# Kernel tuning notes

Hardware: AMD Instinct MI355X
Metric: run time of the kernel (lower is better)

## Reference

```python
import jax, jax.numpy as jnp
import numpy as np

B, C, K = 16384, 10, 5   # batch, context window (2*window_size), num_neg per context
V, D = 400000, 300       # vocab size, embedding dim


def setup_inputs() -> dict:
    key = jax.random.key(0)
    k1, k2, k3, k4, k5 = jax.random.split(key, 5)
    return {
        "target": jax.random.randint(k1, (B,), 0, V, dtype=jnp.int64)
        if jax.config.jax_enable_x64 else jax.random.randint(k1, (B,), 0, V).astype(jnp.int32),
        "context": jax.random.randint(k2, (B, C), 0, V).astype(jnp.int32),
        "negative_samples": jax.random.randint(k3, (B, C * K), 0, V).astype(jnp.int32),
        "emb_in": jax.random.normal(k4, (V, D), dtype=jnp.float32),
        "emb_out": jax.random.normal(k5, (V, D), dtype=jnp.float32),
    }


def reference(target, context, negative_samples, emb_in, emb_out):
    # Skip-gram NCE loss (Word2VecPy.loss).
    tgt = emb_in[target]               # [B, D]
    ctx = emb_out[context]             # [B, C, D]
    neg = emb_out[negative_samples]    # [B, C*K, D]

    # positive: log sigmoid(ctx . tgt), mean over context
    pos_scores = jnp.einsum("bcd,bd->bc", ctx, tgt)          # [B, C]
    pos_loss = jnp.mean(jax.nn.log_sigmoid(pos_scores), axis=1)  # [B]

    # negative: log sigmoid(-neg . tgt), sum over K negatives, mean over context
    neg_scores = -jnp.einsum("bnd,bd->bn", neg, tgt)         # [B, C*K]
    neg_ls = jax.nn.log_sigmoid(neg_scores).reshape(B, C, K)  # [B, C, K]
    neg_loss = jnp.mean(jnp.sum(neg_ls, axis=2), axis=1)      # [B]

    return -jnp.mean(pos_loss + neg_loss)
```

## Files before the change

### kernel.cpp

```cpp
#include <hip/hip_runtime.h>
#include <hip/hip_bf16.h>


#define D_DIM 300
#define D4    75
#define C_DIM 10
#define NEG_DIM 50
#define ROWS 60

__device__ __forceinline__ float log_sigmoid_fast(float x) {
    float e = __expf(-fabsf(x));
    return fminf(x, 0.f) - __logf(1.f + e);
}

__global__ __launch_bounds__(256) void w2v_loss_partial(
    const int*   __restrict__ target,
    const int*   __restrict__ context,
    const int*   __restrict__ negs,
    const float* __restrict__ emb_in,
    const float* __restrict__ emb_out,
    float*       __restrict__ partial)
{
    const int b    = blockIdx.x;
    const int tid  = threadIdx.x;
    const int lane = tid & 63;
    const int wave = tid >> 6;

    __shared__ int   s_idx[ROWS + 4];
    __shared__ float s_acc[4];

    if (tid < C_DIM)       s_idx[tid] = context[b * C_DIM + tid];
    else if (tid < ROWS)   s_idx[tid] = negs[b * NEG_DIM + (tid - C_DIM)];
    __syncthreads();

    const float4* trow =
        reinterpret_cast<const float4*>(emb_in + (size_t)target[b] * D_DIM);
    float4 ta = trow[lane];
    float4 tb = make_float4(0.f, 0.f, 0.f, 0.f);
    if (lane < D4 - 64) tb = trow[64 + lane];

    float acc = 0.f;
    #pragma unroll 3
    for (int rr = 0; rr < ROWS / 4; ++rr) {
        const int r   = wave + rr * 4;
        const int idx = s_idx[r];
        const float4* row =
            reinterpret_cast<const float4*>(emb_out + (size_t)idx * D_DIM);
        float4 ra = row[lane];
        float4 rb = make_float4(0.f, 0.f, 0.f, 0.f);
        if (lane < D4 - 64) rb = row[64 + lane];

        float dot = ra.x * ta.x + ra.y * ta.y + ra.z * ta.z + ra.w * ta.w
                  + rb.x * tb.x + rb.y * tb.y + rb.z * tb.z + rb.w * tb.w;

        #pragma unroll
        for (int off = 32; off > 0; off >>= 1)
            dot += __shfl_xor(dot, off, 64);

        const float x = (r < C_DIM) ? dot : -dot;
        acc += log_sigmoid_fast(x);
    }

    if (lane == 0) s_acc[wave] = acc;
    __syncthreads();
    if (tid == 0) partial[b] = s_acc[0] + s_acc[1] + s_acc[2] + s_acc[3];
}

__global__ __launch_bounds__(256) void w2v_loss_reduce(
    const float* __restrict__ partial,
    float*       __restrict__ out,
    int n, float inv_scale)
{
    __shared__ float s[256];
    float acc = 0.f;
    for (int i = threadIdx.x; i < n; i += 256) acc += partial[i];
    s[threadIdx.x] = acc;
    __syncthreads();
    #pragma unroll
    for (int off = 128; off > 0; off >>= 1) {
        if (threadIdx.x < off) s[threadIdx.x] += s[threadIdx.x + off];
        __syncthreads();
    }
    if (threadIdx.x == 0) out[0] = -s[0] * inv_scale;
}

extern "C" void kernel_launch(void* const* d_in, const int* in_sizes, int n_in,
                              void* d_out, int out_size, void* d_ws, size_t ws_size,
                              hipStream_t stream) {
    const int*   target  = (const int*)  d_in[0];
    const int*   context = (const int*)  d_in[1];
    const int*   negs    = (const int*)  d_in[2];
    const float* emb_in  = (const float*)d_in[3];
    const float* emb_out = (const float*)d_in[4];
    float*       out     = (float*)d_out;

    const int B = in_sizes[0];
    float* partial = (float*)d_ws;

    w2v_loss_partial<<<B, 256, 0, stream>>>(target, context, negs,
                                            emb_in, emb_out, partial);
    const float inv_scale = 1.0f / ((float)B * (float)C_DIM);
    w2v_loss_reduce<<<1, 256, 0, stream>>>(partial, out, B, inv_scale);
}
```

Before: 210.6 us.

## Map one batch item per wave and batch shuffle reductions across four rows

Each wavefront now processes a whole batch item, with four items per block, instead of splitting one item's rows across four waves. Context and negative indices are held in lane registers and broadcast with readlane, which removes the shared-memory staging and block barriers. Four dot products are reduced together with a combined butterfly, cutting the shuffle count per row. The trade-off is more independent loads per wave and a slightly more intricate lane-to-row mapping.

```diff
diff --git a/kernel.cpp b/kernel.cpp
--- a/kernel.cpp
+++ b/kernel.cpp
@@ -21,49 +21,61 @@
     const float* __restrict__ emb_out,
     float*       __restrict__ partial)
 {
-    const int b    = blockIdx.x;
     const int tid  = threadIdx.x;
     const int lane = tid & 63;
     const int wave = tid >> 6;
+    const int b    = blockIdx.x * 4 + wave;
 
-    __shared__ int   s_idx[ROWS + 4];
-    __shared__ float s_acc[4];
-
-    if (tid < C_DIM)       s_idx[tid] = context[b * C_DIM + tid];
-    else if (tid < ROWS)   s_idx[tid] = negs[b * NEG_DIM + (tid - C_DIM)];
-    __syncthreads();
+    int v_idx = 0;
+    if (lane < C_DIM)      v_idx = context[b * C_DIM + lane];
+    else if (lane < ROWS)  v_idx = negs[b * NEG_DIM + (lane - C_DIM)];
 
     const float4* trow =
         reinterpret_cast<const float4*>(emb_in + (size_t)target[b] * D_DIM);
+    const bool tail = lane < (D4 - 64);
     float4 ta = trow[lane];
     float4 tb = make_float4(0.f, 0.f, 0.f, 0.f);
-    if (lane < D4 - 64) tb = trow[64 + lane];
+    if (tail) tb = trow[64 + lane];
 
     float acc = 0.f;
     #pragma unroll 3
-    for (int rr = 0; rr < ROWS / 4; ++rr) {
-        const int r   = wave + rr * 4;
-        const int idx = s_idx[r];
-        const float4* row =
-            reinterpret_cast<const float4*>(emb_out + (size_t)idx * D_DIM);
-        float4 ra = row[lane];
-        float4 rb = make_float4(0.f, 0.f, 0.f, 0.f);
-        if (lane < D4 - 64) rb = row[64 + lane];
-
-        float dot = ra.x * ta.x + ra.y * ta.y + ra.z * ta.z + ra.w * ta.w
-                  + rb.x * tb.x + rb.y * tb.y + rb.z * tb.z + rb.w * tb.w;
+    for (int g = 0; g < ROWS / 4; ++g) {
+        float d[4];
+        #pragma unroll
+        for (int i = 0; i < 4; ++i) {
+            const int r = g * 4 + i;
+            const int sidx = __builtin_amdgcn_readlane(v_idx, r);
+            const float4* row =
+                reinterpret_cast<const float4*>(emb_out + (size_t)sidx * D_DIM);
+            float4 ra = row[lane];
+            float4 rb = make_float4(0.f, 0.f, 0.f, 0.f);
+            if (tail) rb = row[64 + lane];
+            d[i] = ra.x * ta.x + ra.y * ta.y + ra.z * ta.z + ra.w * ta.w
+                 + rb.x * tb.x + rb.y * tb.y + rb.z * tb.z + rb.w * tb.w;
+        }
 
         #pragma unroll
-        for (int off = 32; off > 0; off >>= 1)
-            dot += __shfl_xor(dot, off, 64);
+        for (int i = 0; i < 4; ++i) d[i] += __shfl_xor(d[i], 32, 64);
+        const bool hi32 = (lane & 32) != 0;
+        float p = hi32 ? d[1] : d[0];
+        float q = hi32 ? d[3] : d[2];
+        p += __shfl_xor(p, 16, 64);
+        q += __shfl_xor(q, 16, 64);
+        float v = (lane & 16) ? q : p;
+        v += __shfl_xor(v, 8, 64);
+        v += __shfl_xor(v, 4, 64);
+        v += __shfl_xor(v, 2, 64);
+        v += __shfl_xor(v, 1, 64);
 
-        const float x = (r < C_DIM) ? dot : -dot;
+        const int gq  = lane >> 4;
+        const int rid = g * 4 + (((gq & 1) << 1) | (gq >> 1));
+        const float x = (rid < C_DIM) ? v : -v;
         acc += log_sigmoid_fast(x);
     }
 
-    if (lane == 0) s_acc[wave] = acc;
-    __syncthreads();
-    if (tid == 0) partial[b] = s_acc[0] + s_acc[1] + s_acc[2] + s_acc[3];
+    acc += __shfl_xor(acc, 16, 64);
+    acc += __shfl_xor(acc, 32, 64);
+    if (lane == 0) partial[b] = acc;
 }
 
 __global__ __launch_bounds__(256) void w2v_loss_reduce(
@@ -97,8 +109,8 @@
     const int B = in_sizes[0];
     float* partial = (float*)d_ws;
 
-    w2v_loss_partial<<<B, 256, 0, stream>>>(target, context, negs,
-                                            emb_in, emb_out, partial);
+    w2v_loss_partial<<<B / 4, 256, 0, stream>>>(target, context, negs,
+                                                emb_in, emb_out, partial);
     const float inv_scale = 1.0f / ((float)B * (float)C_DIM);
     w2v_loss_reduce<<<1, 256, 0, stream>>>(partial, out, B, inv_scale);
 }
```

After: 209.9 us. Within noise of the previous version (-0.3%).
